# Kernel tuning notes

Hardware: AMD Instinct MI355X
Metric: run time of the kernel (lower is better)

Reference implementation:

```python
import jax, jax.numpy as jnp
import numpy as np

NUM_CLASSES = 1000
EMBED_DIM = 1024
BATCH = 32768
FACTOR = 0.3


def setup_inputs() -> dict:
    key = jax.random.key(0)
    k1, k2, k3 = jax.random.split(key, 3)
    embed = jax.random.normal(k1, (BATCH, EMBED_DIM), dtype=jnp.float32)
    y = jax.random.randint(k2, (BATCH,), 0, NUM_CLASSES, dtype=jnp.int64)
    centroid = jax.random.normal(k3, (NUM_CLASSES, EMBED_DIM), dtype=jnp.float32)
    return {"embed": embed, "y": y, "centroid": centroid}


def reference(embed, y, centroid):
    # Per-class sum of embeddings: equivalent to eye(C)[y].T @ embed,
    # done as a scatter-add (segment_sum) instead of a dense one-hot matmul.
    sums = jax.ops.segment_sum(embed, y, num_segments=NUM_CLASSES)  # [C, D]
    counts = jax.ops.segment_sum(
        jnp.ones((embed.shape[0],), dtype=embed.dtype), y, num_segments=NUM_CLASSES
    )  # [C] == weight.sum(dim=1)
    cur_centroid = sums / counts[:, None]  # per-class mean
    new_centroid = FACTOR * cur_centroid + (1.0 - FACTOR) * centroid
    return new_centroid
```

## Files before the change

### kernel.cpp

```cpp
#include <hip/hip_runtime.h>
#include <hip/hip_bf16.h>


#define BATCH       32768
#define EMBED_DIM   1024
#define NUM_CLASSES 1000
#define FACTOR      0.3f
#define MAXROWS     512

__global__ __launch_bounds__(256) void centroid_kernel(
    const float* __restrict__ embed,
    const int*   __restrict__ y,
    const float* __restrict__ centroid,
    float*       __restrict__ out)
{
    const int c   = blockIdx.x;
    const int tid = threadIdx.x;

    __shared__ int rows[MAXROWS];
    __shared__ int nmatch;

    if (tid == 0) nmatch = 0;
    __syncthreads();

    const int4* y4 = reinterpret_cast<const int4*>(y);
    #pragma unroll 4
    for (int it = 0; it < BATCH / 1024; ++it) {
        const int  i4   = it * 256 + tid;
        const int4 yv   = y4[i4];
        const int  base = i4 * 4;
        if (yv.x == c) { int p = atomicAdd(&nmatch, 1); rows[p] = base + 0; }
        if (yv.y == c) { int p = atomicAdd(&nmatch, 1); rows[p] = base + 1; }
        if (yv.z == c) { int p = atomicAdd(&nmatch, 1); rows[p] = base + 2; }
        if (yv.w == c) { int p = atomicAdd(&nmatch, 1); rows[p] = base + 3; }
    }
    __syncthreads();
    const int m = nmatch;

    const int d = tid * 4;
    float4 acc = make_float4(0.f, 0.f, 0.f, 0.f);

    int j = 0;
    for (; j + 8 <= m; j += 8) {
        const int r0 = rows[j+0], r1 = rows[j+1], r2 = rows[j+2], r3 = rows[j+3];
        const int r4 = rows[j+4], r5 = rows[j+5], r6 = rows[j+6], r7 = rows[j+7];
        const float4 v0 = *reinterpret_cast<const float4*>(embed + (size_t)r0 * EMBED_DIM + d);
        const float4 v1 = *reinterpret_cast<const float4*>(embed + (size_t)r1 * EMBED_DIM + d);
        const float4 v2 = *reinterpret_cast<const float4*>(embed + (size_t)r2 * EMBED_DIM + d);
        const float4 v3 = *reinterpret_cast<const float4*>(embed + (size_t)r3 * EMBED_DIM + d);
        const float4 v4 = *reinterpret_cast<const float4*>(embed + (size_t)r4 * EMBED_DIM + d);
        const float4 v5 = *reinterpret_cast<const float4*>(embed + (size_t)r5 * EMBED_DIM + d);
        const float4 v6 = *reinterpret_cast<const float4*>(embed + (size_t)r6 * EMBED_DIM + d);
        const float4 v7 = *reinterpret_cast<const float4*>(embed + (size_t)r7 * EMBED_DIM + d);
        acc.x += v0.x + v1.x + v2.x + v3.x + v4.x + v5.x + v6.x + v7.x;
        acc.y += v0.y + v1.y + v2.y + v3.y + v4.y + v5.y + v6.y + v7.y;
        acc.z += v0.z + v1.z + v2.z + v3.z + v4.z + v5.z + v6.z + v7.z;
        acc.w += v0.w + v1.w + v2.w + v3.w + v4.w + v5.w + v6.w + v7.w;
    }
    for (; j < m; ++j) {
        const int r = rows[j];
        const float4 v = *reinterpret_cast<const float4*>(embed + (size_t)r * EMBED_DIM + d);
        acc.x += v.x; acc.y += v.y; acc.z += v.z; acc.w += v.w;
    }

    const float inv = 1.0f / (float)m;
    const size_t o  = (size_t)c * EMBED_DIM + d;
    const float4 cen = *reinterpret_cast<const float4*>(centroid + o);
    float4 res;
    res.x = FACTOR * (acc.x * inv) + (1.0f - FACTOR) * cen.x;
    res.y = FACTOR * (acc.y * inv) + (1.0f - FACTOR) * cen.y;
    res.z = FACTOR * (acc.z * inv) + (1.0f - FACTOR) * cen.z;
    res.w = FACTOR * (acc.w * inv) + (1.0f - FACTOR) * cen.w;
    *reinterpret_cast<float4*>(out + o) = res;
}

extern "C" void kernel_launch(void* const* d_in, const int* in_sizes, int n_in,
                              void* d_out, int out_size, void* d_ws, size_t ws_size,
                              hipStream_t stream) {
    const float* embed    = (const float*)d_in[0];
    const int*   y        = (const int*)d_in[1];
    const float* centroid = (const float*)d_in[2];
    float*       out      = (float*)d_out;

    centroid_kernel<<<NUM_CLASSES, 256, 0, stream>>>(embed, y, centroid, out);
}
```

Before: 213.7 us.

## Replace per-class label scan with counting-sort bucketing pipeline

Before, every one of the 1000 blocks scanned the entire label array (32768 entries) to find its rows, which multiplies label reads by the number of classes. The new version builds a bucketed index: a histogram kernel with global atomics, a single-block prefix scan, and a scatter kernel that writes row indices into per-class segments. The gather kernel then reads its rows directly from that ordered list. This adds four extra launches, a memset and global atomic contention, and the row order inside each class is no longer deterministic, which can change float summation order.

```diff
diff --git a/kernel.cpp b/kernel.cpp
--- a/kernel.cpp
+++ b/kernel.cpp
@@ -6,40 +6,58 @@
 #define EMBED_DIM   1024
 #define NUM_CLASSES 1000
 #define FACTOR      0.3f
-#define MAXROWS     512
 
-__global__ __launch_bounds__(256) void centroid_kernel(
-    const float* __restrict__ embed,
-    const int*   __restrict__ y,
-    const float* __restrict__ centroid,
-    float*       __restrict__ out)
-{
+__global__ __launch_bounds__(256) void k1_count(const int* __restrict__ y,
+                                                int* __restrict__ counts) {
+    const int i = blockIdx.x * 256 + threadIdx.x;
+    atomicAdd(&counts[y[i]], 1);
+}
+
+__global__ __launch_bounds__(1024) void k2_scan(const int* __restrict__ counts,
+                                                int* __restrict__ offsets,
+                                                int* __restrict__ cursor) {
+    __shared__ int s[1024];
+    const int t = threadIdx.x;
+    int v = (t < NUM_CLASSES) ? counts[t] : 0;
+    s[t] = v;
+    __syncthreads();
+    #pragma unroll
+    for (int d = 1; d < 1024; d <<= 1) {
+        int add = (t >= d) ? s[t - d] : 0;
+        __syncthreads();
+        s[t] += add;
+        __syncthreads();
+    }
+    const int excl = s[t] - v;
+    if (t < NUM_CLASSES) {
+        offsets[t] = excl;
+        cursor[t]  = excl;
+    }
+}
+
+__global__ __launch_bounds__(256) void k3_scatter(const int* __restrict__ y,
+                                                  int* __restrict__ cursor,
+                                                  int* __restrict__ order) {
+    const int i = blockIdx.x * 256 + threadIdx.x;
+    const int p = atomicAdd(&cursor[y[i]], 1);
+    order[p] = i;
+}
+
+__global__ __launch_bounds__(256) void k4_gather(const float* __restrict__ embed,
+                                                 const float* __restrict__ centroid,
+                                                 const int* __restrict__ counts,
+                                                 const int* __restrict__ offsets,
+                                                 const int* __restrict__ order,
+                                                 float* __restrict__ out) {
     const int c   = blockIdx.x;
     const int tid = threadIdx.x;
+    const int d   = tid * 4;
 
-    __shared__ int rows[MAXROWS];
-    __shared__ int nmatch;
+    const int m    = counts[c];
+    const int base = offsets[c];
+    const int* __restrict__ rows = order + base;
 
-    if (tid == 0) nmatch = 0;
-    __syncthreads();
-
-    const int4* y4 = reinterpret_cast<const int4*>(y);
-    #pragma unroll 4
-    for (int it = 0; it < BATCH / 1024; ++it) {
-        const int  i4   = it * 256 + tid;
-        const int4 yv   = y4[i4];
-        const int  base = i4 * 4;
-        if (yv.x == c) { int p = atomicAdd(&nmatch, 1); rows[p] = base + 0; }
-        if (yv.y == c) { int p = atomicAdd(&nmatch, 1); rows[p] = base + 1; }
-        if (yv.z == c) { int p = atomicAdd(&nmatch, 1); rows[p] = base + 2; }
-        if (yv.w == c) { int p = atomicAdd(&nmatch, 1); rows[p] = base + 3; }
-    }
-    __syncthreads();
-    const int m = nmatch;
-
-    const int d = tid * 4;
     float4 acc = make_float4(0.f, 0.f, 0.f, 0.f);
-
     int j = 0;
     for (; j + 8 <= m; j += 8) {
         const int r0 = rows[j+0], r1 = rows[j+1], r2 = rows[j+2], r3 = rows[j+3];
@@ -82,5 +100,14 @@
     const float* centroid = (const float*)d_in[2];
     float*       out      = (float*)d_out;
 
-    centroid_kernel<<<NUM_CLASSES, 256, 0, stream>>>(embed, y, centroid, out);
+    int* counts  = (int*)d_ws;
+    int* offsets = counts + 1024;
+    int* cursor  = offsets + 1024;
+    int* order   = cursor + 1024;
+
+    hipMemsetAsync(counts, 0, 1024 * sizeof(int), stream);
+    k1_count  <<<BATCH / 256, 256, 0, stream>>>(y, counts);
+    k2_scan   <<<1, 1024, 0, stream>>>(counts, offsets, cursor);
+    k3_scatter<<<BATCH / 256, 256, 0, stream>>>(y, cursor, order);
+    k4_gather <<<NUM_CLASSES, 256, 0, stream>>>(embed, centroid, counts, offsets, order, out);
 }
```

New measurement: 220.2 us. 3.0% more time.
